# Performance work log

Hardware: AMD Instinct MI355X
Metric: run time of the kernel (lower is better)

Reference implementation:

```python
import jax, jax.numpy as jnp
import numpy as np

EMBED_DIM = 256
MAX_SENT_NUM = 50


def position_embeddings(max_sent_num, embed_dim):
    # pos[p, i] = sin(p / 200**(i/embed_dim))
    p = jnp.arange(max_sent_num, dtype=jnp.float32)[:, None]
    i = jnp.arange(embed_dim, dtype=jnp.float32)[None, :] / embed_dim
    return jnp.sin(p / jnp.power(200.0, i))


def setup_inputs() -> dict:
    key = jax.random.key(0)
    k1, k2, k3, k4 = jax.random.split(key, 4)
    B, S, N, E = 8192, 50, 20, EMBED_DIM
    return {
        "encoded_sents": jax.random.normal(k1, (B, S, E), dtype=jnp.float32),
        "entities": jax.random.normal(k2, (B, N, E), dtype=jnp.float32),
        "attn_matrix": jax.random.normal(k3, (E, E), dtype=jnp.float32) * 0.05,
        "dense_w": jax.random.normal(k4, (E, 1), dtype=jnp.float32) * 0.05,
        "dense_b": jnp.zeros((1,), dtype=jnp.float32),
    }


def reference(encoded_sents, entities, attn_matrix, dense_w, dense_b):
    B, S, E = encoded_sents.shape
    pos = position_embeddings(MAX_SENT_NUM, E)[:S]          # [S, E]
    x = encoded_sents + pos[None, :, :]                      # [B, S, E]

    # attention over previous sentences; query = last sentence's hidden state
    query = x[:, -1, :]                                      # [B, E]
    logits = jnp.einsum("be,bse->bs", query, x)              # [B, S]
    coef = jax.nn.softmax(logits, axis=1)                    # [B, S]
    attn_hidden = jnp.einsum("bs,bse->be", coef, x)          # [B, E]

    # entity attention: (query @ W) elementwise-weighted sum over entities (no softmax)
    q_ent = attn_hidden @ attn_matrix                        # [B, E]
    attn_ent = jnp.einsum("be,bne->be", q_ent, entities)     # [B, E] (sum over n)

    return jax.nn.sigmoid(attn_ent @ dense_w + dense_b)      # [B, 1]
```

## Files before the change

kernel.cpp:

```cpp
#include <hip/hip_runtime.h>
#include <math.h>

#define BATCH 8192
#define SENTS 50
#define ED    256
#define NENT  20
#define BB    16

#define RATE_K 0.0298588132413075f

__global__ __launch_bounds__(512, 8) void attn_ent_kernel(
    const float* __restrict__ sents, const float* __restrict__ entities,
    const float* __restrict__ dense_w,
    float* __restrict__ h_out, float* __restrict__ m_out)
{
    __shared__ float lgp[SENTS][2];
    __shared__ __align__(8) float hpart[4][ED];
    __shared__ __align__(8) float epart[4][ED];

    int t  = threadIdx.x;
    int b  = blockIdx.x;
    int c  = t & 63;
    int sr = t >> 6;
    int r  = sr >> 1;
    int h  = sr & 1;
    int cp = 64 * h + c;

    const float2* s2 = (const float2*)(sents + (size_t)b * SENTS * ED);
    const float2* e2 = (const float2*)(entities + (size_t)b * NENT * ED);

    bool has13 = (r < 2);

    float2 xv[13];
    #pragma unroll
    for (int k = 0; k < 12; ++k) xv[k] = s2[(r + 4 * k) * 128 + cp];
    float2 qsv = s2[49 * 128 + cp];
    float2 ev0 = e2[(r     ) * 128 + cp];
    float2 ev1 = e2[(r +  4) * 128 + cp];
    float2 ev2 = e2[(r +  8) * 128 + cp];
    float2 ev3 = e2[(r + 12) * 128 + cp];
    float2 ev4 = e2[(r + 16) * 128 + cp];
    if (has13) xv[12] = s2[(r + 48) * 128 + cp];

    float rx = exp2f(-(float)(2 * cp + 0) * RATE_K);
    float ry = exp2f(-(float)(2 * cp + 1) * RATE_K);

    float2 q;
    q.x = qsv.x + __sinf(49.f * rx);
    q.y = qsv.y + __sinf(49.f * ry);

    float2 es;
    es.x = ((ev0.x + ev1.x) + (ev2.x + ev3.x)) + ev4.x;
    es.y = ((ev0.y + ev1.y) + (ev2.y + ev3.y)) + ev4.y;

    float2 x[13];
    #pragma unroll
    for (int k = 0; k < 13; ++k) {
        if (k < 12 || has13) {
            float fs = (float)(r + 4 * k);
            x[k].x = xv[k].x + __sinf(fs * rx);
            x[k].y = xv[k].y + __sinf(fs * ry);
            float p = x[k].x * q.x + x[k].y * q.y;
            p += __shfl_xor(p, 1);
            p += __shfl_xor(p, 2);
            p += __shfl_xor(p, 4);
            p += __shfl_xor(p, 8);
            p += __shfl_xor(p, 16);
            p += __shfl_xor(p, 32);
            if (c == 0) lgp[r + 4 * k][h] = p;
        } else {
            x[k] = make_float2(0.f, 0.f);
        }
    }
    __syncthreads();

    float lg = (c < SENTS) ? (lgp[c][0] + lgp[c][1]) : -INFINITY;
    float mx = lg;
    mx = fmaxf(mx, __shfl_xor(mx, 1));
    mx = fmaxf(mx, __shfl_xor(mx, 2));
    mx = fmaxf(mx, __shfl_xor(mx, 4));
    mx = fmaxf(mx, __shfl_xor(mx, 8));
    mx = fmaxf(mx, __shfl_xor(mx, 16));
    mx = fmaxf(mx, __shfl_xor(mx, 32));
    float ex = (c < SENTS) ? __expf(lg - mx) : 0.f;
    float sm = ex;
    sm += __shfl_xor(sm, 1);
    sm += __shfl_xor(sm, 2);
    sm += __shfl_xor(sm, 4);
    sm += __shfl_xor(sm, 8);
    sm += __shfl_xor(sm, 16);
    sm += __shfl_xor(sm, 32);
    float coef = ex / sm;

    float2 hacc = make_float2(0.f, 0.f);
    #pragma unroll
    for (int k = 0; k < 13; ++k) {
        if (k < 12 || has13) {
            float cf = __shfl(coef, r + 4 * k);
            hacc.x += cf * x[k].x;
            hacc.y += cf * x[k].y;
        }
    }
    ((float2*)&hpart[r][2 * cp])[0] = hacc;
    ((float2*)&epart[r][2 * cp])[0] = es;
    __syncthreads();

    if (t < ED) {
        int e = t;
        float v = hpart[0][e] + hpart[1][e] + hpart[2][e] + hpart[3][e];
        h_out[(size_t)b * ED + e] = v;
    } else {
        int e = t - ED;
        float v = epart[0][e] + epart[1][e] + epart[2][e] + epart[3][e];
        m_out[(size_t)b * ED + e] = v * dense_w[e];
    }
}

__global__ __launch_bounds__(256) void bilinear_kernel(
    const float* __restrict__ hws, const float* __restrict__ mws,
    const float* __restrict__ A, const float* __restrict__ dense_b,
    float* __restrict__ out)
{
    __shared__ __align__(16) float hl[BB][ED];
    __shared__ float ml[BB][ED];
    __shared__ float part[BB][ED];

    int t  = threadIdx.x;
    int b0 = blockIdx.x * BB;

    for (int i = 0; i < BB; ++i) {
        hl[i][t] = hws[(size_t)(b0 + i) * ED + t];
        ml[i][t] = mws[(size_t)(b0 + i) * ED + t];
    }
    __syncthreads();

    float acc[BB];
    #pragma unroll
    for (int i = 0; i < BB; ++i) acc[i] = 0.f;

    for (int ep = 0; ep < ED; ep += 4) {
        float a0 = A[(ep + 0) * ED + t];
        float a1 = A[(ep + 1) * ED + t];
        float a2 = A[(ep + 2) * ED + t];
        float a3 = A[(ep + 3) * ED + t];
        #pragma unroll
        for (int i = 0; i < BB; ++i) {
            float4 hv = *(const float4*)&hl[i][ep];
            acc[i] += hv.x * a0 + hv.y * a1 + hv.z * a2 + hv.w * a3;
        }
    }

    #pragma unroll
    for (int i = 0; i < BB; ++i) part[i][t] = acc[i] * ml[i][t];
    __syncthreads();

    int lane = t & 63, w = t >> 6;
    float bias = dense_b[0];
    for (int i = w; i < BB; i += 4) {
        float v = part[i][lane] + part[i][lane + 64] + part[i][lane + 128] + part[i][lane + 192];
        for (int off = 32; off >= 1; off >>= 1) v += __shfl_xor(v, off);
        if (lane == 0) out[b0 + i] = 1.f / (1.f + expf(-(v + bias)));
    }
}

__global__ __launch_bounds__(256) void fused_kernel(
    const float* __restrict__ sents, const float* __restrict__ entities,
    const float* __restrict__ A, const float* __restrict__ dense_w,
    const float* __restrict__ dense_b, float* __restrict__ out)
{
    __shared__ __align__(16) float xs[SENTS][ED + 4];
    __shared__ float logit_s[64];
    __shared__ float coef[64];
    __shared__ __align__(16) float harr[ED];
    __shared__ float marr[ED];
    __shared__ float red[4];

    int t    = threadIdx.x;
    int b    = blockIdx.x;
    int lane = t & 63;
    int w    = t >> 6;

    float rate = exp2f(-(float)t * RATE_K);
    const float* sp = sents + (size_t)b * SENTS * ED;
    for (int s = 0; s < SENTS; ++s)
        xs[s][t] = sp[s * ED + t] + sinf((float)s * rate);
    __syncthreads();

    float4 q = *(const float4*)&xs[SENTS - 1][lane * 4];
    for (int s = w; s < SENTS; s += 4) {
        float4 v = *(const float4*)&xs[s][lane * 4];
        float p = v.x * q.x + v.y * q.y + v.z * q.z + v.w * q.w;
        p += __shfl_down(p, 32);
        p += __shfl_down(p, 16);
        p += __shfl_down(p, 8);
        p += __shfl_down(p, 4);
        p += __shfl_down(p, 2);
        p += __shfl_down(p, 1);
        if (lane == 0) logit_s[s] = p;
    }
    __syncthreads();

    if (w == 0) {
        float l = (lane < SENTS) ? logit_s[lane] : -INFINITY;
        float mx = l;
        for (int off = 32; off >= 1; off >>= 1) mx = fmaxf(mx, __shfl_xor(mx, off));
        float ex = (lane < SENTS) ? expf(l - mx) : 0.f;
        float sm = ex;
        for (int off = 32; off >= 1; off >>= 1) sm += __shfl_xor(sm, off);
        if (lane < SENTS) coef[lane] = ex / sm;
    }
    __syncthreads();

    float h = 0.f;
    #pragma unroll
    for (int s = 0; s < SENTS; ++s) h += coef[s] * xs[s][t];

    const float* ent = entities + (size_t)b * NENT * ED;
    float es = 0.f;
    #pragma unroll
    for (int n = 0; n < NENT; ++n) es += ent[n * ED + t];
    float m = es * dense_w[t];

    harr[t] = h;
    marr[t] = m;
    __syncthreads();

    float acc = 0.f;
    for (int ep = 0; ep < ED; ep += 4) {
        float4 hv = *(const float4*)&harr[ep];
        acc += hv.x * A[(ep + 0) * ED + t];
        acc += hv.y * A[(ep + 1) * ED + t];
        acc += hv.z * A[(ep + 2) * ED + t];
        acc += hv.w * A[(ep + 3) * ED + t];
    }
    float val = acc * marr[t];
    val += __shfl_down(val, 32);
    val += __shfl_down(val, 16);
    val += __shfl_down(val, 8);
    val += __shfl_down(val, 4);
    val += __shfl_down(val, 2);
    val += __shfl_down(val, 1);
    if (lane == 0) red[w] = val;
    __syncthreads();
    if (t == 0) {
        float tot = red[0] + red[1] + red[2] + red[3];
        out[b] = 1.f / (1.f + expf(-(tot + dense_b[0])));
    }
}

extern "C" void kernel_launch(void* const* d_in, const int* in_sizes, int n_in,
                              void* d_out, int out_size, void* d_ws, size_t ws_size,
                              hipStream_t stream) {
    const float* sents    = (const float*)d_in[0];
    const float* entities = (const float*)d_in[1];
    const float* A        = (const float*)d_in[2];
    const float* dense_w  = (const float*)d_in[3];
    const float* dense_b  = (const float*)d_in[4];
    float* out = (float*)d_out;

    size_t hm_bytes = (size_t)BATCH * ED * sizeof(float);
    size_t need = 2 * hm_bytes;

    if (ws_size >= need) {
        float* hws = (float*)d_ws;
        float* mws = (float*)((char*)d_ws + hm_bytes);
        attn_ent_kernel<<<BATCH, 512, 0, stream>>>(sents, entities, dense_w, hws, mws);
        bilinear_kernel<<<BATCH / BB, 256, 0, stream>>>(hws, mws, A, dense_b, out);
    } else {
        fused_kernel<<<BATCH, 256, 0, stream>>>(sents, entities, A, dense_w, dense_b, out);
    }
}
```

Baseline: 149.4 us.

## Reassociate bilinear form: project entity vector through A before sentence attention

The computation is reordered algebraically. The entity sum times dense_w is first multiplied by A^T to give a per-batch vector v, and the sentence kernel then computes the softmax-weighted sum of x·v directly, so h never has to be materialized. The single attention+entity kernel is split into four: an A transpose, an entity reduction, a batched matvec, and the sentence attention that emits the sigmoid. The aim is to remove the hidden-state workspace round trip and the large partial buffers in the bilinear stage. In exchange it adds extra launches and an extra pass over a [B,E] workspace.

```diff
diff --git a/kernel.cpp b/kernel.cpp
--- a/kernel.cpp
+++ b/kernel.cpp
@@ -9,72 +9,140 @@
 
 #define RATE_K 0.0298588132413075f
 
-__global__ __launch_bounds__(512, 8) void attn_ent_kernel(
-    const float* __restrict__ sents, const float* __restrict__ entities,
-    const float* __restrict__ dense_w,
-    float* __restrict__ h_out, float* __restrict__ m_out)
-{
-    __shared__ float lgp[SENTS][2];
-    __shared__ __align__(8) float hpart[4][ED];
-    __shared__ __align__(8) float epart[4][ED];
-
+__global__ __launch_bounds__(256) void at_kernel(
+    const float* __restrict__ A, float* __restrict__ AT)
+{
+    __shared__ float tile[16][17];
     int t  = threadIdx.x;
-    int b  = blockIdx.x;
-    int c  = t & 63;
-    int sr = t >> 6;
-    int r  = sr >> 1;
-    int h  = sr & 1;
-    int cp = 64 * h + c;
-
-    const float2* s2 = (const float2*)(sents + (size_t)b * SENTS * ED);
-    const float2* e2 = (const float2*)(entities + (size_t)b * NENT * ED);
-
+    int tx = t & 15, ty = t >> 4;
+    int bi = blockIdx.x & 15, bj = blockIdx.x >> 4;
+
+    tile[ty][tx] = A[(bi * 16 + ty) * ED + (bj * 16 + tx)];
+    __syncthreads();
+    AT[(bj * 16 + ty) * ED + (bi * 16 + tx)] = tile[tx][ty];
+}
+
+__global__ __launch_bounds__(256) void ent_kernel(
+    const float* __restrict__ entities, const float* __restrict__ dense_w,
+    float* __restrict__ m_out)
+{
+    int t = threadIdx.x;
+    int b = blockIdx.x * 4 + (t >> 6);
+    int c = t & 63;
+
+    const float4* e4 = (const float4*)(entities + (size_t)b * NENT * ED);
+
+    float4 a[NENT];
+    #pragma unroll
+    for (int n = 0; n < NENT; ++n) a[n] = e4[n * 64 + c];
+
+    float4 s = make_float4(0.f, 0.f, 0.f, 0.f);
+    #pragma unroll
+    for (int n = 0; n < NENT; ++n) {
+        s.x += a[n].x; s.y += a[n].y; s.z += a[n].z; s.w += a[n].w;
+    }
+
+    float4 w4 = ((const float4*)dense_w)[c];
+    s.x *= w4.x; s.y *= w4.y; s.z *= w4.z; s.w *= w4.w;
+    ((float4*)(m_out + (size_t)b * ED))[c] = s;
+}
+
+__global__ __launch_bounds__(256) void matvec_kernel(
+    const float* __restrict__ mws, const float* __restrict__ AT,
+    float* __restrict__ vws)
+{
+    __shared__ __align__(16) float ml[BB][ED];
+
+    int t  = threadIdx.x;
+    int b0 = blockIdx.x * BB;
+
+    for (int i = 0; i < BB; ++i)
+        ml[i][t] = mws[(size_t)(b0 + i) * ED + t];
+    __syncthreads();
+
+    float acc[BB];
+    #pragma unroll
+    for (int i = 0; i < BB; ++i) acc[i] = 0.f;
+
+    for (int e = 0; e < ED; e += 4) {
+        float a0 = AT[(e + 0) * ED + t];
+        float a1 = AT[(e + 1) * ED + t];
+        float a2 = AT[(e + 2) * ED + t];
+        float a3 = AT[(e + 3) * ED + t];
+        #pragma unroll
+        for (int i = 0; i < BB; ++i) {
+            float4 mv = *(const float4*)&ml[i][e];
+            acc[i] += mv.x * a0 + mv.y * a1 + mv.z * a2 + mv.w * a3;
+        }
+    }
+
+    #pragma unroll
+    for (int i = 0; i < BB; ++i)
+        vws[(size_t)(b0 + i) * ED + t] = acc[i];
+}
+
+__global__ __launch_bounds__(256) void sents_kernel(
+    const float* __restrict__ sents, const float* __restrict__ vws,
+    const float* __restrict__ dense_b, float* __restrict__ out)
+{
+    __shared__ float lgs[64];
+    __shared__ float wred[4];
+
+    int t = threadIdx.x;
+    int c = t & 63;
+    int r = t >> 6;
+    int b = blockIdx.x;
     bool has13 = (r < 2);
 
-    float2 xv[13];
-    #pragma unroll
-    for (int k = 0; k < 12; ++k) xv[k] = s2[(r + 4 * k) * 128 + cp];
-    float2 qsv = s2[49 * 128 + cp];
-    float2 ev0 = e2[(r     ) * 128 + cp];
-    float2 ev1 = e2[(r +  4) * 128 + cp];
-    float2 ev2 = e2[(r +  8) * 128 + cp];
-    float2 ev3 = e2[(r + 12) * 128 + cp];
-    float2 ev4 = e2[(r + 16) * 128 + cp];
-    if (has13) xv[12] = s2[(r + 48) * 128 + cp];
-
-    float rx = exp2f(-(float)(2 * cp + 0) * RATE_K);
-    float ry = exp2f(-(float)(2 * cp + 1) * RATE_K);
-
-    float2 q;
-    q.x = qsv.x + __sinf(49.f * rx);
-    q.y = qsv.y + __sinf(49.f * ry);
-
-    float2 es;
-    es.x = ((ev0.x + ev1.x) + (ev2.x + ev3.x)) + ev4.x;
-    es.y = ((ev0.y + ev1.y) + (ev2.y + ev3.y)) + ev4.y;
-
-    float2 x[13];
+    const float4* s4 = (const float4*)(sents + (size_t)b * SENTS * ED);
+
+    float4 qv = s4[49 * 64 + c];
+    float4 vv = ((const float4*)(vws + (size_t)b * ED))[c];
+    float4 xv[13];
+    #pragma unroll
+    for (int k = 0; k < 12; ++k) xv[k] = s4[(r + 4 * k) * 64 + c];
+    if (has13) xv[12] = s4[(r + 48) * 64 + c];
+
+    float4 rate;
+    rate.x = exp2f(-(float)(4 * c + 0) * RATE_K);
+    rate.y = exp2f(-(float)(4 * c + 1) * RATE_K);
+    rate.z = exp2f(-(float)(4 * c + 2) * RATE_K);
+    rate.w = exp2f(-(float)(4 * c + 3) * RATE_K);
+
+    float4 q;
+    q.x = qv.x + __sinf(49.f * rate.x);
+    q.y = qv.y + __sinf(49.f * rate.y);
+    q.z = qv.z + __sinf(49.f * rate.z);
+    q.w = qv.w + __sinf(49.f * rate.w);
+
+    float zp[13];
     #pragma unroll
     for (int k = 0; k < 13; ++k) {
         if (k < 12 || has13) {
             float fs = (float)(r + 4 * k);
-            x[k].x = xv[k].x + __sinf(fs * rx);
-            x[k].y = xv[k].y + __sinf(fs * ry);
-            float p = x[k].x * q.x + x[k].y * q.y;
+            float4 x;
+            x.x = xv[k].x + __sinf(fs * rate.x);
+            x.y = xv[k].y + __sinf(fs * rate.y);
+            x.z = xv[k].z + __sinf(fs * rate.z);
+            x.w = xv[k].w + __sinf(fs * rate.w);
+
+            zp[k] = x.x * vv.x + x.y * vv.y + x.z * vv.z + x.w * vv.w;
+
+            float p = x.x * q.x + x.y * q.y + x.z * q.z + x.w * q.w;
             p += __shfl_xor(p, 1);
             p += __shfl_xor(p, 2);
             p += __shfl_xor(p, 4);
             p += __shfl_xor(p, 8);
             p += __shfl_xor(p, 16);
             p += __shfl_xor(p, 32);
-            if (c == 0) lgp[r + 4 * k][h] = p;
+            if (c == 0) lgs[r + 4 * k] = p;
         } else {
-            x[k] = make_float2(0.f, 0.f);
+            zp[k] = 0.f;
         }
     }
     __syncthreads();
 
-    float lg = (c < SENTS) ? (lgp[c][0] + lgp[c][1]) : -INFINITY;
+    float lg = (c < SENTS) ? lgs[c] : -INFINITY;
     float mx = lg;
     mx = fmaxf(mx, __shfl_xor(mx, 1));
     mx = fmaxf(mx, __shfl_xor(mx, 2));
@@ -92,74 +160,24 @@
     sm += __shfl_xor(sm, 32);
     float coef = ex / sm;
 
-    float2 hacc = make_float2(0.f, 0.f);
+    float acc = 0.f;
     #pragma unroll
     for (int k = 0; k < 13; ++k) {
-        if (k < 12 || has13) {
-            float cf = __shfl(coef, r + 4 * k);
-            hacc.x += cf * x[k].x;
-            hacc.y += cf * x[k].y;
-        }
-    }
-    ((float2*)&hpart[r][2 * cp])[0] = hacc;
-    ((float2*)&epart[r][2 * cp])[0] = es;
-    __syncthreads();
-
-    if (t < ED) {
-        int e = t;
-        float v = hpart[0][e] + hpart[1][e] + hpart[2][e] + hpart[3][e];
-        h_out[(size_t)b * ED + e] = v;
-    } else {
-        int e = t - ED;
-        float v = epart[0][e] + epart[1][e] + epart[2][e] + epart[3][e];
-        m_out[(size_t)b * ED + e] = v * dense_w[e];
-    }
-}
-
-__global__ __launch_bounds__(256) void bilinear_kernel(
-    const float* __restrict__ hws, const float* __restrict__ mws,
-    const float* __restrict__ A, const float* __restrict__ dense_b,
-    float* __restrict__ out)
-{
-    __shared__ __align__(16) float hl[BB][ED];
-    __shared__ float ml[BB][ED];
-    __shared__ float part[BB][ED];
-
-    int t  = threadIdx.x;
-    int b0 = blockIdx.x * BB;
-
-    for (int i = 0; i < BB; ++i) {
-        hl[i][t] = hws[(size_t)(b0 + i) * ED + t];
-        ml[i][t] = mws[(size_t)(b0 + i) * ED + t];
-    }
-    __syncthreads();
-
-    float acc[BB];
-    #pragma unroll
-    for (int i = 0; i < BB; ++i) acc[i] = 0.f;
-
-    for (int ep = 0; ep < ED; ep += 4) {
-        float a0 = A[(ep + 0) * ED + t];
-        float a1 = A[(ep + 1) * ED + t];
-        float a2 = A[(ep + 2) * ED + t];
-        float a3 = A[(ep + 3) * ED + t];
-        #pragma unroll
-        for (int i = 0; i < BB; ++i) {
-            float4 hv = *(const float4*)&hl[i][ep];
-            acc[i] += hv.x * a0 + hv.y * a1 + hv.z * a2 + hv.w * a3;
-        }
-    }
-
-    #pragma unroll
-    for (int i = 0; i < BB; ++i) part[i][t] = acc[i] * ml[i][t];
-    __syncthreads();
-
-    int lane = t & 63, w = t >> 6;
-    float bias = dense_b[0];
-    for (int i = w; i < BB; i += 4) {
-        float v = part[i][lane] + part[i][lane + 64] + part[i][lane + 128] + part[i][lane + 192];
-        for (int off = 32; off >= 1; off >>= 1) v += __shfl_xor(v, off);
-        if (lane == 0) out[b0 + i] = 1.f / (1.f + expf(-(v + bias)));
+        if (k < 12 || has13)
+            acc += __shfl(coef, r + 4 * k) * zp[k];
+    }
+    acc += __shfl_xor(acc, 1);
+    acc += __shfl_xor(acc, 2);
+    acc += __shfl_xor(acc, 4);
+    acc += __shfl_xor(acc, 8);
+    acc += __shfl_xor(acc, 16);
+    acc += __shfl_xor(acc, 32);
+    if (c == 0) wred[r] = acc;
+    __syncthreads();
+
+    if (t == 0) {
+        float tot = (wred[0] + wred[1]) + (wred[2] + wred[3]);
+        out[b] = 1.f / (1.f + __expf(-(tot + dense_b[0])));
     }
 }
 
@@ -259,13 +277,17 @@
     float* out = (float*)d_out;
 
     size_t hm_bytes = (size_t)BATCH * ED * sizeof(float);
-    size_t need = 2 * hm_bytes;
+    size_t at_bytes = (size_t)ED * ED * sizeof(float);
+    size_t need = 2 * hm_bytes + at_bytes;
 
     if (ws_size >= need) {
-        float* hws = (float*)d_ws;
-        float* mws = (float*)((char*)d_ws + hm_bytes);
-        attn_ent_kernel<<<BATCH, 512, 0, stream>>>(sents, entities, dense_w, hws, mws);
-        bilinear_kernel<<<BATCH / BB, 256, 0, stream>>>(hws, mws, A, dense_b, out);
+        float* mws = (float*)d_ws;
+        float* vws = (float*)((char*)d_ws + hm_bytes);
+        float* ATw = (float*)((char*)d_ws + 2 * hm_bytes);
+        at_kernel<<<256, 256, 0, stream>>>(A, ATw);
+        ent_kernel<<<BATCH / 4, 256, 0, stream>>>(entities, dense_w, mws);
+        matvec_kernel<<<BATCH / BB, 256, 0, stream>>>(mws, ATw, vws);
+        sents_kernel<<<BATCH, 256, 0, stream>>>(sents, vws, dense_b, out);
     } else {
         fused_kernel<<<BATCH, 256, 0, stream>>>(sents, entities, A, dense_w, dense_b, out);
     }
```

Result: faster. 143.8 us (-3.8%).
